# Optimization experiments

Hardware: AMD Instinct MI355X
Metric: run time of the kernel (lower is better)

Reference implementation:

```python
import jax, jax.numpy as jnp
import numpy as np

# Static problem sizes
B, TMAX = 32, 48                 # subjects, max windows per subject
NPW, NWIN = 128, 1024            # nodes per window, total windows (= sum(lengths))
EPW = 2048                       # edges per window (avg degree 16)
N, E = NWIN * NPW, NWIN * EPW    # 131072 nodes, 2097152 edges
IN_DIM, GNN_H, GRU_H = 128, 128, 128


def setup_inputs() -> dict:
    key = jax.random.key(0)
    ks = jax.random.split(key, 12)
    x = jax.random.normal(ks[0], (N, IN_DIM), jnp.float32)
    # random intra-window edges: endpoints within each window's 128-node block
    base = jax.random.randint(ks[1], (2, NWIN, EPW), 0, NPW)
    offs = (jnp.arange(NWIN) * NPW)[None, :, None]
    edge_index = (base + offs).reshape(2, E)
    batch_idx = jnp.repeat(jnp.arange(NWIN), NPW)          # node -> window id
    lengths = jnp.asarray(np.tile([16, 48], B // 2), jnp.int32)  # sums to NWIN
    s = 0.05
    p = lambda k, shape: jax.random.normal(k, shape, jnp.float32) * s
    return dict(
        x=x, edge_index=edge_index, batch_idx=batch_idx, lengths=lengths,
        # GIN layer 1 MLP (weights stored [in,out])
        w1a=p(ks[2], (IN_DIM, GNN_H)), b1a=jnp.zeros((GNN_H,), jnp.float32),
        w1b=p(ks[3], (GNN_H, GNN_H)), b1b=jnp.zeros((GNN_H,), jnp.float32),
        # GIN layer 2 MLP
        w2a=p(ks[4], (GNN_H, GNN_H)), b2a=jnp.zeros((GNN_H,), jnp.float32),
        w2b=p(ks[5], (GNN_H, GNN_H)), b2b=jnp.zeros((GNN_H,), jnp.float32),
        # GRU (torch layout: [3H, in], gate order r,z,n)
        wih=p(ks[6], (3 * GRU_H, GNN_H)), whh=p(ks[7], (3 * GRU_H, GRU_H)),
        bih=jnp.zeros((3 * GRU_H,), jnp.float32), bhh=jnp.zeros((3 * GRU_H,), jnp.float32),
        # output head
        wout=p(ks[8], (GRU_H, 1)), bout=jnp.zeros((1,), jnp.float32),
    )


def _gin(h, src, dst, wa, ba, wb, bb):
    # GINConv with eps=0: mlp(x + sum_{j->i} x_j)
    aggr = jax.ops.segment_sum(h[src], dst, num_segments=N)
    z = h + aggr
    z = jax.nn.relu(z @ wa + ba)
    return z @ wb + bb


def _forward(x, w1a, b1a, w1b, b1b, w2a, b2a, w2b, b2b,
             wih, whh, bih, bhh, wout, bout, edge_index, batch_idx, lengths):
    src, dst = edge_index[0], edge_index[1]
    h = jax.nn.relu(_gin(x, src, dst, w1a, b1a, w1b, b1b))
    h = jax.nn.relu(_gin(h, src, dst, w2a, b2a, w2b, b2b))
    # global mean pool per window -> [NWIN, GNN_H]
    sums = jax.ops.segment_sum(h, batch_idx, num_segments=NWIN)
    cnt = jax.ops.segment_sum(jnp.ones((N, 1), h.dtype), batch_idx, num_segments=NWIN)
    g = sums / cnt
    # pad_sequence: scatter flat window embeddings into [B, TMAX, H]
    csum = jnp.cumsum(lengths)
    starts = jnp.concatenate([jnp.zeros((1,), lengths.dtype), csum[:-1]])
    win_ids = jnp.arange(NWIN)
    subj = jnp.searchsorted(csum, win_ids, side='right')
    pos = win_ids - starts[subj]
    padded = jnp.zeros((B, TMAX, GNN_H), g.dtype).at[subj, pos].set(g)
    # masked GRU == pack_padded_sequence semantics (state frozen past length)
    mask = jnp.arange(TMAX)[:, None] < lengths[None, :]   # [T, B]
    xs = jnp.swapaxes(padded, 0, 1)                        # [T, B, H]

    def step(hc, inputs):
        xt, mt = inputs
        gx = xt @ wih.T + bih
        gh = hc @ whh.T + bhh
        rx, zx, nx = jnp.split(gx, 3, axis=-1)
        rh, zh, nh = jnp.split(gh, 3, axis=-1)
        r = jax.nn.sigmoid(rx + rh)
        z = jax.nn.sigmoid(zx + zh)
        n = jnp.tanh(nx + r * nh)
        hn = (1 - z) * n + z * hc
        hn = jnp.where(mt[:, None], hn, hc)
        return hn, None

    h0 = jnp.zeros((B, GRU_H), g.dtype)
    h_last, _ = jax.lax.scan(step, h0, (xs, mask))
    return (h_last @ wout + bout).squeeze(-1)  # [B]


def reference(x, edge_index, batch_idx, lengths,
              w1a, b1a, w1b, b1b, w2a, b2a, w2b, b2b,
              wih, whh, bih, bhh, wout, bout):
    return _forward(x, w1a, b1a, w1b, b1b, w2a, b2a, w2b, b2b,
                    wih, whh, bih, bhh, wout, bout, edge_index, batch_idx, lengths)
```

## Files before the change

kernel.cpp:

```cpp
#include <hip/hip_runtime.h>
#include <hip/hip_bf16.h>
#include <stdint.h>

#define NPW   128
#define NWIN  1024
#define EPW   2048
#define NEDGE (NWIN * EPW)
#define BSUBJ 32
#define TMAXW 48

typedef __bf16 bf16x8_t __attribute__((ext_vector_type(8)));
typedef float  f32x4_t  __attribute__((ext_vector_type(4)));

#define B1_OFF   0
#define B2_OFF   32768
#define B3_OFF   65536
#define BIAS_OFF 98304
#define GP_OFF   100352
#define K1_LDS   100864

__device__ __forceinline__ int swzb(int row, int col ) {
  return row * 256 + ((col * 2) ^ ((row & 7) << 4));
}

__device__ __forceinline__ void stage_wT(const float* __restrict__ wsrc, char* B3, int tid) {
  const int k = tid >> 2, o0 = (tid & 3) * 32;
  const float4* src = (const float4*)(wsrc + k * 128 + o0);
  #pragma unroll
  for (int c = 0; c < 8; ++c) {
    float4 v = src[c];
    int o = o0 + c * 4;
    *(__bf16*)(B3 + swzb(o + 0, k)) = (__bf16)v.x;
    *(__bf16*)(B3 + swzb(o + 1, k)) = (__bf16)v.y;
    *(__bf16*)(B3 + swzb(o + 2, k)) = (__bf16)v.z;
    *(__bf16*)(B3 + swzb(o + 3, k)) = (__bf16)v.w;
  }
}

__device__ __forceinline__ void gemm_acc(const char* Ab, const char* Bb, int lane, int rt,
                                         f32x4_t acc[8]) {
  const int rowA = rt * 16 + (lane & 15);
  const int k8 = (lane >> 4) * 8;
  const int swA = (rowA & 7) << 4;
  const int swB = ((lane & 7)) << 4;
  #pragma unroll
  for (int kk = 0; kk < 4; ++kk) {
    const int kb = (kk * 32 + k8) * 2;
    bf16x8_t af = *(const bf16x8_t*)(Ab + rowA * 256 + (kb ^ swA));
    #pragma unroll
    for (int ct = 0; ct < 8; ++ct) {
      const int rowB = ct * 16 + (lane & 15);
      bf16x8_t bv = *(const bf16x8_t*)(Bb + rowB * 256 + (kb ^ swB));
      acc[ct] = __builtin_amdgcn_mfma_f32_16x16x32_bf16(af, bv, acc[ct], 0, 0, 0);
    }
  }
}

__device__ __forceinline__ void write_row(char* Dst, int lane, int rt, const f32x4_t acc[8],
                                          const float* bias, bool relu) {
  const int r0 = rt * 16 + (lane >> 4) * 4;
  const int c = lane & 15;
  #pragma unroll
  for (int ct = 0; ct < 8; ++ct) {
    const int col = ct * 16 + c;
    const float bvl = bias ? bias[col] : 0.f;
    #pragma unroll
    for (int j = 0; j < 4; ++j) {
      float v = acc[ct][j] + bvl;
      if (relu) v = fmaxf(v, 0.f);
      *(__bf16*)(Dst + swzb(r0 + j, col)) = (__bf16)v;
    }
  }
}

__device__ __forceinline__ void write_transposed(char* Dst, int lane, int rt, const f32x4_t acc[8],
                                                 const float* bias, bool relu) {
  const int r0 = rt * 16 + (lane >> 4) * 4;
  const int c = lane & 15;
  #pragma unroll
  for (int ct = 0; ct < 8; ++ct) {
    const int col = ct * 16 + c;
    const float bvl = bias ? bias[col] : 0.f;
    unsigned long long pk = 0ull;
    #pragma unroll
    for (int j = 0; j < 4; ++j) {
      float v = acc[ct][j] + bvl;
      if (relu) v = fmaxf(v, 0.f);
      unsigned short u = __builtin_bit_cast(unsigned short, (__bf16)v);
      pk |= ((unsigned long long)u) << (16 * j);
    }
    *(unsigned long long*)(Dst + col * 256 + ((r0 * 2) ^ ((col & 7) << 4))) = pk;
  }
}

__global__ void __launch_bounds__(512)
gin_gnn_kernel(const float* __restrict__ x, const int* __restrict__ ei,
               const float* __restrict__ w1a, const float* __restrict__ b1a,
               const float* __restrict__ w1b, const float* __restrict__ b1b,
               const float* __restrict__ w2a, const float* __restrict__ b2a,
               const float* __restrict__ w2b, const float* __restrict__ b2b,
               float* __restrict__ g_out) {
  extern __shared__ __align__(16) char sm[];
  const int w = blockIdx.x;
  const int tid = threadIdx.x;
  const int lane = tid & 63;
  const int wv = tid >> 6;

  unsigned* M32 = (unsigned*)(sm + B1_OFF);
  float* gp = (float*)(sm + GP_OFF);
  float* biasb = (float*)(sm + BIAS_OFF);
  char* B1 = sm + B1_OFF;
  char* B2 = sm + B2_OFF;
  char* B3 = sm + B3_OFF;

  #pragma unroll
  for (int i = tid; i < 8192; i += 512) M32[i] = 0u;
  if (tid < 128) gp[tid] = 0.f;
  __syncthreads();

  {
    const int base = w * EPW;
    #pragma unroll
    for (int rr = 0; rr < 4; ++rr) {
      const int e = base + tid + rr * 512;
      const int s = ei[e] & 127;
      const int d = ei[NEDGE + e] & 127;
      atomicAdd(&M32[(d << 6) + (s >> 1)], 1u << ((s & 1) * 16));
    }
  }
  {
    const int i = tid >> 2, f0 = (tid & 3) * 32;
    const float4* src = (const float4*)(x + ((size_t)w * 128 + i) * 128 + f0);
    #pragma unroll
    for (int c = 0; c < 8; ++c) {
      float4 v = src[c];
      const int f = f0 + c * 4;
      *(__bf16*)(B2 + swzb(f + 0, i)) = (__bf16)v.x;
      *(__bf16*)(B2 + swzb(f + 1, i)) = (__bf16)v.y;
      *(__bf16*)(B2 + swzb(f + 2, i)) = (__bf16)v.z;
      *(__bf16*)(B2 + swzb(f + 3, i)) = (__bf16)v.w;
    }
  }
  {
    const float* bp = (tid < 128) ? b1a : (tid < 256) ? b1b : (tid < 384) ? b2a : b2b;
    biasb[tid] = bp[tid & 127];
  }
  stage_wT(w1a, B3, tid);
  __syncthreads();

  {
    unsigned mv[16];
    #pragma unroll
    for (int c = 0; c < 16; ++c) mv[c] = M32[tid * 16 + c];
    __syncthreads();
    #pragma unroll
    for (int c = 0; c < 16; ++c) {
      const int idx = tid * 16 + c;
      const int d = idx >> 6;
      const int s0 = (idx & 63) * 2;
      unsigned c0 = mv[c] & 0xffffu, c1 = mv[c] >> 16;
      if (d == s0) ++c0;
      if (d == s0 + 1) ++c1;
      const unsigned short p0 = __builtin_bit_cast(unsigned short, (__bf16)(float)c0);
      const unsigned short p1 = __builtin_bit_cast(unsigned short, (__bf16)(float)c1);
      *(unsigned*)(B1 + d * 256 + ((s0 * 2) ^ ((d & 7) << 4))) = (unsigned)p0 | ((unsigned)p1 << 16);
    }
  }
  __syncthreads();

  f32x4_t acc[8];
  #define ZACC() { _Pragma("unroll") for (int q = 0; q < 8; ++q) acc[q] = (f32x4_t){0.f,0.f,0.f,0.f}; }

  ZACC(); gemm_acc(B1, B2, lane, wv, acc); __syncthreads();
  write_row(B2, lane, wv, acc, nullptr, false); __syncthreads();
  ZACC(); gemm_acc(B2, B3, lane, wv, acc); __syncthreads();
  write_row(B2, lane, wv, acc, biasb + 0, true);
  stage_wT(w1b, B3, tid); __syncthreads();
  ZACC(); gemm_acc(B2, B3, lane, wv, acc); __syncthreads();
  write_transposed(B2, lane, wv, acc, biasb + 128, true);
  stage_wT(w2a, B3, tid); __syncthreads();
  ZACC(); gemm_acc(B1, B2, lane, wv, acc); __syncthreads();
  write_row(B2, lane, wv, acc, nullptr, false); __syncthreads();
  ZACC(); gemm_acc(B2, B3, lane, wv, acc); __syncthreads();
  write_row(B2, lane, wv, acc, biasb + 256, true);
  stage_wT(w2b, B3, tid); __syncthreads();
  ZACC(); gemm_acc(B2, B3, lane, wv, acc);
  {
    const int c = lane & 15;
    #pragma unroll
    for (int ct = 0; ct < 8; ++ct) {
      const int col = ct * 16 + c;
      const float bvl = biasb[384 + col];
      float s = 0.f;
      #pragma unroll
      for (int j = 0; j < 4; ++j) s += fmaxf(acc[ct][j] + bvl, 0.f);
      s += __shfl_xor(s, 16);
      s += __shfl_xor(s, 32);
      if (lane < 16) atomicAdd(&gp[col], s);
    }
  }
  __syncthreads();
  if (tid < 128) g_out[(size_t)w * 128 + tid] = gp[tid] * (1.f / 128.f);
}

__global__ void __launch_bounds__(384)
gx_kernel(const float* __restrict__ g, const float* __restrict__ wih,
          const float* __restrict__ bih, const int* __restrict__ lengths,
          float* __restrict__ GX) {
  __shared__ float gt[16][128];
  __shared__ int sps[16], spp[16];
  const int w0 = blockIdx.x * 16;
  const int tid = threadIdx.x;
  for (int i = tid; i < 2048; i += 384) gt[i >> 7][i & 127] = g[(size_t)w0 * 128 + i];
  if (tid < 16) {
    const int w = w0 + tid;
    int s = 0, start = 0;
    #pragma unroll 1
    for (int b = 0; b < BSUBJ; ++b) {
      const int L = lengths[b];
      if (w >= start + L) { start += L; ++s; } else break;
    }
    sps[tid] = s;
    spp[tid] = w - start;
  }
  __syncthreads();
  const int o = tid;
  float accw[16];
  #pragma unroll
  for (int i = 0; i < 16; ++i) accw[i] = 0.f;
  for (int k0 = 0; k0 < 128; k0 += 4) {
    const float4 wv = *(const float4*)(wih + (size_t)o * 128 + k0);
    #pragma unroll
    for (int ww = 0; ww < 16; ++ww)
      accw[ww] += wv.x * gt[ww][k0] + wv.y * gt[ww][k0 + 1] +
                  wv.z * gt[ww][k0 + 2] + wv.w * gt[ww][k0 + 3];
  }
  const float bo = bih[o];
  #pragma unroll
  for (int ww = 0; ww < 16; ++ww)
    GX[((size_t)sps[ww] * TMAXW + spp[ww]) * 384 + o] = accw[ww] + bo;
}

__global__ void __launch_bounds__(384)
gru_kernel(const float* __restrict__ GX, const float* __restrict__ whh,
           const float* __restrict__ bhh, const float* __restrict__ wout,
           const float* __restrict__ bout, const int* __restrict__ lengths,
           float* __restrict__ outp) {
  __shared__ float hb[128], rb[128], zb[128], nb[128];
  const int b = blockIdx.x;
  const int o = threadIdx.x;
  const int lane = o & 63;

  float wrf[128];
  {
    const float* wr = whh + (size_t)o * 128;
    #pragma unroll
    for (int q = 0; q < 32; ++q) {
      float4 v = ((const float4*)wr)[q];
      wrf[4 * q + 0] = v.x; wrf[4 * q + 1] = v.y;
      wrf[4 * q + 2] = v.z; wrf[4 * q + 3] = v.w;
    }
  }
  if (o < 128) hb[o] = 0.f;
  const float bho = bhh[o];
  const float wouto = (o < 128) ? wout[o] : 0.f;
  const int len = lengths[b];
  __syncthreads();

  for (int t = 0; t < len; ++t) {
    const float2 hv = *(const float2*)(hb + 2 * lane);
    float acc = 0.f;
    #pragma unroll
    for (int k2 = 0; k2 < 64; ++k2) {
      const float h0 = __builtin_bit_cast(float,
          __builtin_amdgcn_readlane(__builtin_bit_cast(int, hv.x), k2));
      const float h1 = __builtin_bit_cast(float,
          __builtin_amdgcn_readlane(__builtin_bit_cast(int, hv.y), k2));
      acc = fmaf(wrf[2 * k2], h0, acc);
      acc = fmaf(wrf[2 * k2 + 1], h1, acc);
    }
    const float gh = acc + bho;
    const float gx = GX[((size_t)b * TMAXW + t) * 384 + o];
    if (o < 256) {
      const float v = 1.f / (1.f + __expf(-(gx + gh)));
      if (o < 128) rb[o] = v; else zb[o - 128] = v;
    }
    __syncthreads();
    if (o >= 256) {
      const float pre = gx + rb[o - 256] * gh;
      const float e2 = __expf(-2.f * pre);
      nb[o - 256] = (1.f - e2) / (1.f + e2);
    }
    __syncthreads();
    if (o < 128) {
      const float z = zb[o];
      hb[o] = (1.f - z) * nb[o] + z * hb[o];
    }
    __syncthreads();
  }

  if (o < 128) rb[o] = hb[o] * wouto;
  __syncthreads();
  if (o == 0) {
    float s = 0.f;
    for (int f = 0; f < 128; ++f) s += rb[f];
    outp[b] = s + bout[0];
  }
}

extern "C" void kernel_launch(void* const* d_in, const int* in_sizes, int n_in,
                              void* d_out, int out_size, void* d_ws, size_t ws_size,
                              hipStream_t stream) {
  const float* x    = (const float*)d_in[0];
  const int*   ei   = (const int*)d_in[1];
  const int*   len  = (const int*)d_in[3];
  const float* w1a  = (const float*)d_in[4];
  const float* b1a  = (const float*)d_in[5];
  const float* w1b  = (const float*)d_in[6];
  const float* b1b  = (const float*)d_in[7];
  const float* w2a  = (const float*)d_in[8];
  const float* b2a  = (const float*)d_in[9];
  const float* w2b  = (const float*)d_in[10];
  const float* b2b  = (const float*)d_in[11];
  const float* wih  = (const float*)d_in[12];
  const float* whh  = (const float*)d_in[13];
  const float* bih  = (const float*)d_in[14];
  const float* bhh  = (const float*)d_in[15];
  const float* wout = (const float*)d_in[16];
  const float* bout = (const float*)d_in[17];

  float* g  = (float*)d_ws;
  float* GX = (float*)((char*)d_ws + (size_t)NWIN * 128 * 4);

  hipLaunchKernelGGL(gin_gnn_kernel, dim3(NWIN), dim3(512), K1_LDS, stream,
                     x, ei, w1a, b1a, w1b, b1b, w2a, b2a, w2b, b2b, g);
  hipLaunchKernelGGL(gx_kernel, dim3(NWIN / 16), dim3(384), 0, stream,
                     g, wih, bih, len, GX);
  hipLaunchKernelGGL(gru_kernel, dim3(BSUBJ), dim3(384), 0, stream,
                     GX, whh, bhh, wout, bout, len, (float*)d_out);
}
```

Baseline: 312.0 us.

## Pre-transpose GIN weights to bf16 once and stream them from global

Adds a small prep kernel that converts the four GIN MLP weight matrices to transposed bf16 once per launch. The GNN kernel then reads weight fragments straight from global/L2 instead of restaging them into LDS for every window. This shrinks LDS per block from about 100KB to about 68KB, so more blocks can be resident per CU, and it drops the per-block weight conversion and its barriers. It also widens the swizzle to 16 rows, vectorizes the x and adjacency staging writes, and changes the GRU matvec to read broadcast float4 values from LDS instead of using readlane, with a wave-shuffle reduction for the output. The cost is one extra kernel launch and weight operands that now come from cache rather than LDS.

```diff
diff --git a/kernel.cpp b/kernel.cpp
--- a/kernel.cpp
+++ b/kernel.cpp
@@ -14,38 +14,26 @@
 
 #define B1_OFF   0
 #define B2_OFF   32768
-#define B3_OFF   65536
-#define BIAS_OFF 98304
-#define GP_OFF   100352
-#define K1_LDS   100864
-
-__device__ __forceinline__ int swzb(int row, int col ) {
-  return row * 256 + ((col * 2) ^ ((row & 7) << 4));
-}
-
-__device__ __forceinline__ void stage_wT(const float* __restrict__ wsrc, char* B3, int tid) {
-  const int k = tid >> 2, o0 = (tid & 3) * 32;
-  const float4* src = (const float4*)(wsrc + k * 128 + o0);
-  #pragma unroll
-  for (int c = 0; c < 8; ++c) {
-    float4 v = src[c];
-    int o = o0 + c * 4;
-    *(__bf16*)(B3 + swzb(o + 0, k)) = (__bf16)v.x;
-    *(__bf16*)(B3 + swzb(o + 1, k)) = (__bf16)v.y;
-    *(__bf16*)(B3 + swzb(o + 2, k)) = (__bf16)v.z;
-    *(__bf16*)(B3 + swzb(o + 3, k)) = (__bf16)v.w;
-  }
-}
-
-__device__ __forceinline__ void gemm_acc(const char* Ab, const char* Bb, int lane, int rt,
+#define BIAS_OFF 65536
+#define GP_OFF   67584
+#define K1_LDS   68096
+
+__device__ __forceinline__ unsigned short bfbits(float v) {
+  return __builtin_bit_cast(unsigned short, (__bf16)v);
+}
+
+__device__ __forceinline__ int swz(int row, int colbyte) {
+  return row * 256 + (colbyte ^ ((row & 15) << 4));
+}
+
+__device__ __forceinline__ void gemm_lds(const char* Ab, const char* Bb, int lane, int rt,
                                          f32x4_t acc[8]) {
   const int rowA = rt * 16 + (lane & 15);
-  const int k8 = (lane >> 4) * 8;
-  const int swA = (rowA & 7) << 4;
-  const int swB = ((lane & 7)) << 4;
+  const int swA = (rowA & 15) << 4;
+  const int swB = (lane & 15) << 4;
   #pragma unroll
   for (int kk = 0; kk < 4; ++kk) {
-    const int kb = (kk * 32 + k8) * 2;
+    const int kb = kk * 64 + (lane >> 4) * 16;
     bf16x8_t af = *(const bf16x8_t*)(Ab + rowA * 256 + (kb ^ swA));
     #pragma unroll
     for (int ct = 0; ct < 8; ++ct) {
@@ -56,6 +44,22 @@
   }
 }
 
+__device__ __forceinline__ void gemm_gw(const char* Ab, const __bf16* __restrict__ Wt,
+                                        int lane, int rt, f32x4_t acc[8]) {
+  const int rowA = rt * 16 + (lane & 15);
+  const int swA = (rowA & 15) << 4;
+  #pragma unroll
+  for (int kk = 0; kk < 4; ++kk) {
+    const int ke = kk * 32 + (lane >> 4) * 8;
+    bf16x8_t af = *(const bf16x8_t*)(Ab + rowA * 256 + ((ke * 2) ^ swA));
+    #pragma unroll
+    for (int ct = 0; ct < 8; ++ct) {
+      bf16x8_t bv = *(const bf16x8_t*)(Wt + (size_t)(ct * 16 + (lane & 15)) * 128 + ke);
+      acc[ct] = __builtin_amdgcn_mfma_f32_16x16x32_bf16(af, bv, acc[ct], 0, 0, 0);
+    }
+  }
+}
+
 __device__ __forceinline__ void write_row(char* Dst, int lane, int rt, const f32x4_t acc[8],
                                           const float* bias, bool relu) {
   const int r0 = rt * 16 + (lane >> 4) * 4;
@@ -68,13 +72,13 @@
     for (int j = 0; j < 4; ++j) {
       float v = acc[ct][j] + bvl;
       if (relu) v = fmaxf(v, 0.f);
-      *(__bf16*)(Dst + swzb(r0 + j, col)) = (__bf16)v;
-    }
-  }
-}
-
-__device__ __forceinline__ void write_transposed(char* Dst, int lane, int rt, const f32x4_t acc[8],
-                                                 const float* bias, bool relu) {
+      *(__bf16*)(Dst + swz(r0 + j, col * 2)) = (__bf16)v;
+    }
+  }
+}
+
+__device__ __forceinline__ void write_tr(char* Dst, int lane, int rt, const f32x4_t acc[8],
+                                         const float* bias, bool relu) {
   const int r0 = rt * 16 + (lane >> 4) * 4;
   const int c = lane & 15;
   #pragma unroll
@@ -86,20 +90,33 @@
     for (int j = 0; j < 4; ++j) {
       float v = acc[ct][j] + bvl;
       if (relu) v = fmaxf(v, 0.f);
-      unsigned short u = __builtin_bit_cast(unsigned short, (__bf16)v);
-      pk |= ((unsigned long long)u) << (16 * j);
-    }
-    *(unsigned long long*)(Dst + col * 256 + ((r0 * 2) ^ ((col & 7) << 4))) = pk;
-  }
-}
-
-__global__ void __launch_bounds__(512)
+      pk |= ((unsigned long long)bfbits(v)) << (16 * j);
+    }
+    *(unsigned long long*)(Dst + swz(col, r0 * 2)) = pk;
+  }
+}
+
+__global__ void __launch_bounds__(128)
+wprep_kernel(const float* __restrict__ w1a, const float* __restrict__ w1b,
+             const float* __restrict__ w2a, const float* __restrict__ w2b,
+             __bf16* __restrict__ wt) {
+  const float* srcs[4] = {w1a, w1b, w2a, w2b};
+  const float* src = srcs[blockIdx.x];
+  const int j = threadIdx.x;
+  unsigned* dst = (unsigned*)(wt + (size_t)blockIdx.x * 16384) + j * 64;
+  #pragma unroll 8
+  for (int k2 = 0; k2 < 64; ++k2) {
+    float a = src[(size_t)(2 * k2) * 128 + j];
+    float b = src[(size_t)(2 * k2 + 1) * 128 + j];
+    dst[k2] = (unsigned)bfbits(a) | ((unsigned)bfbits(b) << 16);
+  }
+}
+
+__global__ void __launch_bounds__(512, 4)
 gin_gnn_kernel(const float* __restrict__ x, const int* __restrict__ ei,
-               const float* __restrict__ w1a, const float* __restrict__ b1a,
-               const float* __restrict__ w1b, const float* __restrict__ b1b,
-               const float* __restrict__ w2a, const float* __restrict__ b2a,
-               const float* __restrict__ w2b, const float* __restrict__ b2b,
-               float* __restrict__ g_out) {
+               const float* __restrict__ b1a, const float* __restrict__ b1b,
+               const float* __restrict__ b2a, const float* __restrict__ b2b,
+               const __bf16* __restrict__ wt, float* __restrict__ g_out) {
   extern __shared__ __align__(16) char sm[];
   const int w = blockIdx.x;
   const int tid = threadIdx.x;
@@ -111,7 +128,6 @@
   float* biasb = (float*)(sm + BIAS_OFF);
   char* B1 = sm + B1_OFF;
   char* B2 = sm + B2_OFF;
-  char* B3 = sm + B3_OFF;
 
   #pragma unroll
   for (int i = tid; i < 8192; i += 512) M32[i] = 0u;
@@ -129,41 +145,45 @@
     }
   }
   {
-    const int i = tid >> 2, f0 = (tid & 3) * 32;
-    const float4* src = (const float4*)(x + ((size_t)w * 128 + i) * 128 + f0);
-    #pragma unroll
-    for (int c = 0; c < 8; ++c) {
-      float4 v = src[c];
-      const int f = f0 + c * 4;
-      *(__bf16*)(B2 + swzb(f + 0, i)) = (__bf16)v.x;
-      *(__bf16*)(B2 + swzb(f + 1, i)) = (__bf16)v.y;
-      *(__bf16*)(B2 + swzb(f + 2, i)) = (__bf16)v.z;
-      *(__bf16*)(B2 + swzb(f + 3, i)) = (__bf16)v.w;
+    const int i0 = (tid & 63) * 2, f0 = (tid >> 6) * 16;
+    const float* r0p = x + ((size_t)w * 128 + i0) * 128 + f0;
+    const float* r1p = r0p + 128;
+    float va[16], vb[16];
+    #pragma unroll
+    for (int c = 0; c < 4; ++c) {
+      *(float4*)(va + 4 * c) = *(const float4*)(r0p + 4 * c);
+      *(float4*)(vb + 4 * c) = *(const float4*)(r1p + 4 * c);
+    }
+    #pragma unroll
+    for (int q = 0; q < 16; ++q) {
+      const int f = f0 + q;
+      unsigned pk = (unsigned)bfbits(va[q]) | ((unsigned)bfbits(vb[q]) << 16);
+      *(unsigned*)(B2 + f * 256 + ((4 * (tid & 63)) ^ ((f & 15) << 4))) = pk;
     }
   }
   {
     const float* bp = (tid < 128) ? b1a : (tid < 256) ? b1b : (tid < 384) ? b2a : b2b;
     biasb[tid] = bp[tid & 127];
   }
-  stage_wT(w1a, B3, tid);
-  __syncthreads();
-
-  {
-    unsigned mv[16];
-    #pragma unroll
-    for (int c = 0; c < 16; ++c) mv[c] = M32[tid * 16 + c];
+  __syncthreads();
+
+  {
+    const int d = tid >> 2, bq = tid & 3;
+    const uint4* Mv = (const uint4*)(M32 + d * 64 + bq * 16);
+    uint4 m[4];
+    m[0] = Mv[0]; m[1] = Mv[1]; m[2] = Mv[2]; m[3] = Mv[3];
     __syncthreads();
-    #pragma unroll
-    for (int c = 0; c < 16; ++c) {
-      const int idx = tid * 16 + c;
-      const int d = idx >> 6;
-      const int s0 = (idx & 63) * 2;
-      unsigned c0 = mv[c] & 0xffffu, c1 = mv[c] >> 16;
-      if (d == s0) ++c0;
-      if (d == s0 + 1) ++c1;
-      const unsigned short p0 = __builtin_bit_cast(unsigned short, (__bf16)(float)c0);
-      const unsigned short p1 = __builtin_bit_cast(unsigned short, (__bf16)(float)c1);
-      *(unsigned*)(B1 + d * 256 + ((s0 * 2) ^ ((d & 7) << 4))) = (unsigned)p0 | ((unsigned)p1 << 16);
+    const unsigned* mu = (const unsigned*)m;
+    unsigned* row = (unsigned*)(B1 + d * 256);
+    const int sw = (d & 15) << 4;
+    #pragma unroll
+    for (int q = 0; q < 16; ++q) {
+      const int mi = bq * 16 + q;
+      unsigned c0 = mu[q] & 0xffffu, c1 = mu[q] >> 16;
+      if (d == 2 * mi) ++c0;
+      if (d == 2 * mi + 1) ++c1;
+      row[((4 * mi) ^ sw) >> 2] = (unsigned)bfbits((float)c0) |
+                                  ((unsigned)bfbits((float)c1) << 16);
     }
   }
   __syncthreads();
@@ -171,20 +191,17 @@
   f32x4_t acc[8];
   #define ZACC() { _Pragma("unroll") for (int q = 0; q < 8; ++q) acc[q] = (f32x4_t){0.f,0.f,0.f,0.f}; }
 
-  ZACC(); gemm_acc(B1, B2, lane, wv, acc); __syncthreads();
+  ZACC(); gemm_lds(B1, B2, lane, wv, acc); __syncthreads();
   write_row(B2, lane, wv, acc, nullptr, false); __syncthreads();
-  ZACC(); gemm_acc(B2, B3, lane, wv, acc); __syncthreads();
-  write_row(B2, lane, wv, acc, biasb + 0, true);
-  stage_wT(w1b, B3, tid); __syncthreads();
-  ZACC(); gemm_acc(B2, B3, lane, wv, acc); __syncthreads();
-  write_transposed(B2, lane, wv, acc, biasb + 128, true);
-  stage_wT(w2a, B3, tid); __syncthreads();
-  ZACC(); gemm_acc(B1, B2, lane, wv, acc); __syncthreads();
+  ZACC(); gemm_gw(B2, wt, lane, wv, acc); __syncthreads();
+  write_row(B2, lane, wv, acc, biasb + 0, true); __syncthreads();
+  ZACC(); gemm_gw(B2, wt + 16384, lane, wv, acc); __syncthreads();
+  write_tr(B2, lane, wv, acc, biasb + 128, true); __syncthreads();
+  ZACC(); gemm_lds(B1, B2, lane, wv, acc); __syncthreads();
   write_row(B2, lane, wv, acc, nullptr, false); __syncthreads();
-  ZACC(); gemm_acc(B2, B3, lane, wv, acc); __syncthreads();
-  write_row(B2, lane, wv, acc, biasb + 256, true);
-  stage_wT(w2b, B3, tid); __syncthreads();
-  ZACC(); gemm_acc(B2, B3, lane, wv, acc);
+  ZACC(); gemm_gw(B2, wt + 32768, lane, wv, acc); __syncthreads();
+  write_row(B2, lane, wv, acc, biasb + 256, true); __syncthreads();
+  ZACC(); gemm_gw(B2, wt + 49152, lane, wv, acc);
   {
     const int c = lane & 15;
     #pragma unroll
@@ -246,10 +263,10 @@
            const float* __restrict__ bhh, const float* __restrict__ wout,
            const float* __restrict__ bout, const int* __restrict__ lengths,
            float* __restrict__ outp) {
-  __shared__ float hb[128], rb[128], zb[128], nb[128];
+  __shared__ __align__(16) float hb[128];
+  __shared__ float rb[128], zb[128], nb[128];
   const int b = blockIdx.x;
   const int o = threadIdx.x;
-  const int lane = o & 63;
 
   float wrf[128];
   {
@@ -257,29 +274,31 @@
     #pragma unroll
     for (int q = 0; q < 32; ++q) {
       float4 v = ((const float4*)wr)[q];
-      wrf[4 * q + 0] = v.x; wrf[4 * q + 1] = v.y;
-      wrf[4 * q + 2] = v.z; wrf[4 * q + 3] = v.w;
+      wrf[4*q+0] = v.x; wrf[4*q+1] = v.y; wrf[4*q+2] = v.z; wrf[4*q+3] = v.w;
     }
   }
   if (o < 128) hb[o] = 0.f;
   const float bho = bhh[o];
-  const float wouto = (o < 128) ? wout[o] : 0.f;
   const int len = lengths[b];
   __syncthreads();
 
   for (int t = 0; t < len; ++t) {
-    const float2 hv = *(const float2*)(hb + 2 * lane);
-    float acc = 0.f;
-    #pragma unroll
-    for (int k2 = 0; k2 < 64; ++k2) {
-      const float h0 = __builtin_bit_cast(float,
-          __builtin_amdgcn_readlane(__builtin_bit_cast(int, hv.x), k2));
-      const float h1 = __builtin_bit_cast(float,
-          __builtin_amdgcn_readlane(__builtin_bit_cast(int, hv.y), k2));
-      acc = fmaf(wrf[2 * k2], h0, acc);
-      acc = fmaf(wrf[2 * k2 + 1], h1, acc);
-    }
-    const float gh = acc + bho;
+    float a0 = 0.f, a1 = 0.f, a2 = 0.f, a3 = 0.f;
+    const float4* hv4 = (const float4*)hb;
+    #pragma unroll
+    for (int q = 0; q < 8; ++q) {
+      const float4 h0 = hv4[4*q+0], h1 = hv4[4*q+1], h2 = hv4[4*q+2], h3 = hv4[4*q+3];
+      const float* wq = wrf + 16 * q;
+      a0 = fmaf(wq[0],  h0.x, a0); a0 = fmaf(wq[1],  h0.y, a0);
+      a0 = fmaf(wq[2],  h0.z, a0); a0 = fmaf(wq[3],  h0.w, a0);
+      a1 = fmaf(wq[4],  h1.x, a1); a1 = fmaf(wq[5],  h1.y, a1);
+      a1 = fmaf(wq[6],  h1.z, a1); a1 = fmaf(wq[7],  h1.w, a1);
+      a2 = fmaf(wq[8],  h2.x, a2); a2 = fmaf(wq[9],  h2.y, a2);
+      a2 = fmaf(wq[10], h2.z, a2); a2 = fmaf(wq[11], h2.w, a2);
+      a3 = fmaf(wq[12], h3.x, a3); a3 = fmaf(wq[13], h3.y, a3);
+      a3 = fmaf(wq[14], h3.z, a3); a3 = fmaf(wq[15], h3.w, a3);
+    }
+    const float gh = (a0 + a1) + (a2 + a3) + bho;
     const float gx = GX[((size_t)b * TMAXW + t) * 384 + o];
     if (o < 256) {
       const float v = 1.f / (1.f + __expf(-(gx + gh)));
@@ -299,13 +318,13 @@
     __syncthreads();
   }
 
-  if (o < 128) rb[o] = hb[o] * wouto;
-  __syncthreads();
-  if (o == 0) {
-    float s = 0.f;
-    for (int f = 0; f < 128; ++f) s += rb[f];
-    outp[b] = s + bout[0];
-  }
+  float part = (o < 128) ? hb[o] * wout[o] : 0.f;
+  #pragma unroll
+  for (int d = 1; d < 64; d <<= 1) part += __shfl_xor(part, d);
+  __shared__ float red[6];
+  if ((o & 63) == 0) red[o >> 6] = part;
+  __syncthreads();
+  if (o == 0) outp[b] = red[0] + red[1] + bout[0];
 }
 
 extern "C" void kernel_launch(void* const* d_in, const int* in_sizes, int n_in,
@@ -329,11 +348,14 @@
   const float* wout = (const float*)d_in[16];
   const float* bout = (const float*)d_in[17];
 
-  float* g  = (float*)d_ws;
-  float* GX = (float*)((char*)d_ws + (size_t)NWIN * 128 * 4);
-
+  float*  g  = (float*)d_ws;
+  float*  GX = (float*)((char*)d_ws + (size_t)NWIN * 128 * 4);
+  __bf16* wt = (__bf16*)((char*)d_ws + (size_t)NWIN * 128 * 4
+                         + (size_t)BSUBJ * TMAXW * 384 * 4);
+
+  hipLaunchKernelGGL(wprep_kernel, dim3(4), dim3(128), 0, stream, w1a, w1b, w2a, w2b, wt);
   hipLaunchKernelGGL(gin_gnn_kernel, dim3(NWIN), dim3(512), K1_LDS, stream,
-                     x, ei, w1a, b1a, w1b, b1b, w2a, b2a, w2b, b2b, g);
+                     x, ei, b1a, b1b, b2a, b2b, wt, g);
   hipLaunchKernelGGL(gx_kernel, dim3(NWIN / 16), dim3(384), 0, stream,
                      g, wih, bih, len, GX);
   hipLaunchKernelGGL(gru_kernel, dim3(BSUBJ), dim3(384), 0, stream,
```

New measurement: 338.1 us. 1.08x slower.
